# Kernel tuning notes

Measured on AMD Instinct MI355X. Metric: run time of the kernel, lower is better.

Reference implementation:

```python
import jax, jax.numpy as jnp
import numpy as np

B, E, H, NC = 16384, 1024, 8, 32
FF = 4 * E

def _ln(x, g, b, eps=1e-5):
    m = jnp.mean(x, -1, keepdims=True)
    v = jnp.mean((x - m) ** 2, -1, keepdims=True)
    return (x - m) * jax.lax.rsqrt(v + eps) * g + b

def _mha1(q_in, kv_in, Wq, Wk, Wv, bq, bk, bv, Wo, bo):
    # seq_len == 1 for both query and key/value; x: [B, E]
    Bn = q_in.shape[0]
    dh = E // H
    q = (q_in @ Wq.T + bq).reshape(Bn, H, dh)
    k = (kv_in @ Wk.T + bk).reshape(Bn, H, dh)
    v = (kv_in @ Wv.T + bv).reshape(Bn, H, dh)
    s = jnp.sum(q * k, -1, keepdims=True) / np.float32(np.sqrt(dh))  # [B,H,1]
    w = jax.nn.softmax(s, axis=-1)  # single key -> weights == 1 exactly
    o = (w * v).reshape(Bn, E)
    return o @ Wo.T + bo

def _ffn(x, W1, b1, W2, b2):
    h = jax.nn.gelu(x @ W1.T + b1, approximate=False)  # torch GELU = exact erf
    return h @ W2.T + b2

def setup_inputs():
    key = jax.random.key(0)
    ks = iter(jax.random.split(key, 64))
    def w(shape, s=0.02):
        return jax.random.normal(next(ks), shape, jnp.float32) * s
    z = lambda n: jnp.zeros((n,), jnp.float32)
    o = lambda n: jnp.ones((n,), jnp.float32)
    d = {
        'lc_cls': jax.random.normal(next(ks), (B, E), jnp.float32),
        'tab_embedding': jax.random.normal(next(ks), (B, E), jnp.float32),
        'ln_lc_g': o(E), 'ln_lc_b': z(E),
        'ln_tab_g': o(E), 'ln_tab_b': z(E),
    }
    for p in ('alc', 'atab'):
        d[p + '_Wq'] = w((E, E)); d[p + '_Wk'] = w((E, E)); d[p + '_Wv'] = w((E, E))
        d[p + '_bq'] = z(E); d[p + '_bk'] = z(E); d[p + '_bv'] = z(E)
        d[p + '_Wo'] = w((E, E)); d[p + '_bo'] = z(E)
    for p in ('flc', 'ftab'):
        d[p + '_W1'] = w((FF, E)); d[p + '_b1'] = z(FF)
        d[p + '_W2'] = w((E, FF)); d[p + '_b2'] = z(E)
    d['on_g'] = o(2 * E); d['on_b'] = z(2 * E)
    d['c_W1'] = w((E, 2 * E)); d['c_b1'] = z(E)
    d['c_ln_g'] = o(E); d['c_ln_b'] = z(E)
    d['c_W2'] = w((NC, E)); d['c_b2'] = z(NC)
    return d

def reference(lc_cls, tab_embedding, ln_lc_g, ln_lc_b, ln_tab_g, ln_tab_b,
              alc_Wq, alc_Wk, alc_Wv, alc_bq, alc_bk, alc_bv, alc_Wo, alc_bo,
              atab_Wq, atab_Wk, atab_Wv, atab_bq, atab_bk, atab_bv, atab_Wo, atab_bo,
              flc_W1, flc_b1, flc_W2, flc_b2, ftab_W1, ftab_b1, ftab_W2, ftab_b2,
              on_g, on_b, c_W1, c_b1, c_ln_g, c_ln_b, c_W2, c_b2):
    # dropout is identity at inference
    lc_n = _ln(lc_cls, ln_lc_g, ln_lc_b)
    tab_n = _ln(tab_embedding, ln_tab_g, ln_tab_b)
    lc_cross = lc_cls + _mha1(lc_n, tab_n, alc_Wq, alc_Wk, alc_Wv, alc_bq, alc_bk, alc_bv, alc_Wo, alc_bo)
    tab_cross = tab_embedding + _mha1(tab_n, lc_n, atab_Wq, atab_Wk, atab_Wv, atab_bq, atab_bk, atab_bv, atab_Wo, atab_bo)
    lc_out = lc_cross + _ffn(lc_cross, flc_W1, flc_b1, flc_W2, flc_b2)
    tab_out = tab_cross + _ffn(tab_cross, ftab_W1, ftab_b1, ftab_W2, ftab_b2)
    fused = _ln(jnp.concatenate([lc_out, tab_out], axis=1), on_g, on_b)
    h = jax.nn.gelu(_ln(fused @ c_W1.T + c_b1, c_ln_g, c_ln_b), approximate=False)
    return h @ c_W2.T + c_b2
```

## Files before the change

### kernel.cpp

```cpp
#include <hip/hip_runtime.h>
#include <hip/hip_bf16.h>
#include <math.h>

typedef __bf16 bf16_t;
typedef __bf16 bf16x8 __attribute__((ext_vector_type(8)));
typedef __bf16 bf16x4 __attribute__((ext_vector_type(4)));
typedef float  f32x4  __attribute__((ext_vector_type(4)));

#define NB   16384
#define EDIM 1024
#define FFD  4096
#define NCD  32

__device__ __forceinline__ float gelu_exact(float x) {
    return 0.5f * x * (1.0f + erff(x * 0.70710678118654752f));
}

__device__ __forceinline__ void gload16(const bf16_t* g, bf16_t* l) {
    __builtin_amdgcn_global_load_lds(
        (__attribute__((address_space(1))) void*)(g),
        (__attribute__((address_space(3))) void*)(l),
        16, 0, 0);
}

#define PH_BAR() do { asm volatile("" ::: "memory"); \
                      __builtin_amdgcn_s_barrier();  \
                      asm volatile("" ::: "memory"); } while (0)

enum { EPI_PLAIN = 0, EPI_RESF32 = 1, EPI_GELU = 2, EPI_RESBF16 = 3 };

struct GemmArgs {
    const bf16_t* A0; const bf16_t* A1;
    const bf16_t* B0; const bf16_t* B1;
    const float*  bias0; const float* bias1;
    const void*   res0; const void*  res1;
    bf16_t*       out0; bf16_t*      out1;
};

template<int EPI>
__global__ __launch_bounds__(256, 4)
void gemmDB(GemmArgs g, int ldo, int co0, int co1, int M, int N, int K)
{
    __shared__ __align__(128) bf16_t lds[16384];
    char* const ldsb = (char*)lds;

    const int side = blockIdx.z;
    const bf16_t* __restrict__ A    = side ? g.A1   : g.A0;
    const bf16_t* __restrict__ Bw   = side ? g.B1   : g.B0;
    const float*  __restrict__ bias = side ? g.bias1: g.bias0;
    const void*   __restrict__ resid= side ? g.res1 : g.res0;
    bf16_t*       __restrict__ out  = side ? g.out1 : g.out0;
    const int coloff = side ? co1 : co0;

    const int nx = gridDim.x;
    const int nwg = nx * gridDim.y;
    int lin = blockIdx.y * nx + blockIdx.x;
    {
        const int q = nwg >> 3, r = nwg & 7;
        const int xc = lin & 7, ix = lin >> 3;
        lin = (xc < r ? xc * (q + 1) : r * (q + 1) + (xc - r) * q) + ix;
    }
    const long bm = (long)(lin / nx) * 128;
    const long bn = (long)(lin % nx) * 128;

    const int tid = threadIdx.x, lane = tid & 63, wave = tid >> 6;
    const int wr = (wave >> 1) * 64, wc = (wave & 1) * 64;
    const int fr = lane & 15, ks = lane >> 4;
    const int fx = fr & 3;
    const int csw = (ks ^ fx) << 4;

    const int srow = lane >> 2;
    const int sl   = ((lane & 3) ^ ((lane >> 2) & 3)) * 8;
    auto STAGE = [&](const bf16_t* __restrict__ Mat, long row0, long kt,
                     int dsto) {
        #pragma unroll
        for (int i = 0; i < 2; ++i) {
            gload16(Mat + (row0 + i * 64 + wave * 16 + srow) * (long)K + kt + sl,
                    (bf16_t*)(ldsb + dsto + (i * 256 + wave * 64) * 16));
        }
    };

    f32x4 acc[4][4] = {};
    const int nt = K >> 5;

    STAGE(A,  bm, 0, 0);
    STAGE(Bw, bn, 0, 8192);
    asm volatile("s_waitcnt vmcnt(0)" ::: "memory");
    PH_BAR();

    for (int t = 0; t < nt; ++t) {
        const char* base = ldsb + (t & 1) * 16384;
        bf16x8 av[4], bv[4];
        #pragma unroll
        for (int i = 0; i < 4; ++i) {
            av[i] = *(const bf16x8*)(base + (wr + i * 16 + fr) * 64 + csw);
            bv[i] = *(const bf16x8*)(base + 8192 + (wc + i * 16 + fr) * 64 + csw);
        }
        if (t + 1 < nt) {
            const int nb = ((t + 1) & 1) * 16384;
            STAGE(A,  bm, (long)(t + 1) << 5, nb);
            STAGE(Bw, bn, (long)(t + 1) << 5, nb + 8192);
        }
        #pragma unroll
        for (int mi = 0; mi < 4; ++mi)
            #pragma unroll
            for (int ni = 0; ni < 4; ++ni)
                acc[mi][ni] = __builtin_amdgcn_mfma_f32_16x16x32_bf16(
                                  av[mi], bv[ni], acc[mi][ni], 0, 0, 0);
        asm volatile("s_waitcnt vmcnt(0)" ::: "memory");
        PH_BAR();
    }

    const int rq = (lane >> 4) * 4;
    #pragma unroll
    for (int mi = 0; mi < 4; ++mi) {
        #pragma unroll
        for (int ni = 0; ni < 4; ++ni) {
            const long n = bn + wc + ni * 16 + fr;
            const float bval = bias ? bias[n] : 0.0f;
            #pragma unroll
            for (int r = 0; r < 4; ++r) {
                const long m = bm + wr + mi * 16 + rq + r;
                float v = acc[mi][ni][r] + bval;
                if (EPI == EPI_RESF32)  v += ((const float*)resid)[m * (long)N + n];
                if (EPI == EPI_RESBF16) v += (float)((const bf16_t*)resid)[m * (long)N + n];
                if (EPI == EPI_GELU)    v = gelu_exact(v);
                out[m * (long)ldo + coloff + n] = (bf16_t)v;
            }
        }
    }
}

__global__ __launch_bounds__(256)
void final_mfma(const bf16_t* __restrict__ U, const bf16_t* __restrict__ W2,
                const float* __restrict__ b2, float* __restrict__ out)
{
    __shared__ bf16_t sA[128 * 32];
    __shared__ bf16_t sB[32 * 32];
    const int tid = threadIdx.x, lane = tid & 63, wave = tid >> 6;
    const long bm = (long)blockIdx.x * 128;
    const int srow = lane >> 2, scol = (lane & 3) * 8;

    const bf16_t* gA = U + (bm + wave * 32 + srow) * (long)EDIM + scol;
    bf16_t* lA = sA + wave * 32 * 32;
    const bf16_t* gB = W2 + ((long)wave * 16 + srow) * EDIM + scol;
    bf16_t* lB = sB + wave * 16 * 32;

    const int fr = lane & 15, fk = (lane >> 4) * 8;
    const bf16_t* rA = sA + (wave * 32 + fr) * 32 + fk;
    const bf16_t* rB = sB + fr * 32 + fk;

    f32x4 acc[2][2] = {};
    for (int kt = 0; kt < EDIM; kt += 32) {
        gload16(gA + kt,             lA);
        gload16(gA + kt + 16 * EDIM, lA + 16 * 32);
        if (wave < 2) gload16(gB + kt, lB);
        __syncthreads();
        bf16x8 av[2], bv[2];
        av[0] = *(const bf16x8*)(rA);
        av[1] = *(const bf16x8*)(rA + 16 * 32);
        bv[0] = *(const bf16x8*)(rB);
        bv[1] = *(const bf16x8*)(rB + 16 * 32);
        #pragma unroll
        for (int mi = 0; mi < 2; ++mi)
            #pragma unroll
            for (int ni = 0; ni < 2; ++ni)
                acc[mi][ni] = __builtin_amdgcn_mfma_f32_16x16x32_bf16(
                                  av[mi], bv[ni], acc[mi][ni], 0, 0, 0);
        __syncthreads();
    }
    const int rq = (lane >> 4) * 4;
    #pragma unroll
    for (int mi = 0; mi < 2; ++mi)
        #pragma unroll
        for (int ni = 0; ni < 2; ++ni) {
            const int n = ni * 16 + fr;
            const float bval = b2[n];
            #pragma unroll
            for (int r = 0; r < 4; ++r) {
                const long m = bm + wave * 32 + mi * 16 + rq + r;
                out[m * NCD + n] = acc[mi][ni][r] + bval;
            }
        }
}

__global__ __launch_bounds__(256)
void ln_f32(const float* __restrict__ X, const float* __restrict__ g,
            const float* __restrict__ b, bf16_t* __restrict__ out)
{
    const long row = blockIdx.x;
    const int t = threadIdx.x;
    f32x4 x = ((const f32x4*)(X + row * EDIM))[t];
    float s = x[0] + x[1] + x[2] + x[3];
    float q = x[0]*x[0] + x[1]*x[1] + x[2]*x[2] + x[3]*x[3];
    #pragma unroll
    for (int off = 32; off; off >>= 1) { s += __shfl_xor(s, off); q += __shfl_xor(q, off); }
    __shared__ float red[8];
    if ((t & 63) == 0) { red[(t >> 6) * 2] = s; red[(t >> 6) * 2 + 1] = q; }
    __syncthreads();
    s = red[0] + red[2] + red[4] + red[6];
    q = red[1] + red[3] + red[5] + red[7];
    const float mean = s * (1.0f / EDIM);
    const float rs = rsqrtf(q * (1.0f / EDIM) - mean * mean + 1e-5f);
    f32x4 gg = ((const f32x4*)g)[t];
    f32x4 bb = ((const f32x4*)b)[t];
    bf16x4 o;
    #pragma unroll
    for (int j = 0; j < 4; ++j) o[j] = (bf16_t)((x[j] - mean) * rs * gg[j] + bb[j]);
    ((bf16x4*)(out + row * EDIM))[t] = o;
}

__global__ __launch_bounds__(256)
void ln_cat(const bf16_t* __restrict__ X, const float* __restrict__ g,
            const float* __restrict__ b, bf16_t* __restrict__ out)
{
    const long row = blockIdx.x;
    const int t = threadIdx.x;
    bf16x8 xv = ((const bf16x8*)(X + row * 2048))[t];
    float xf[8];
    float s = 0.f, q = 0.f;
    #pragma unroll
    for (int j = 0; j < 8; ++j) { xf[j] = (float)xv[j]; s += xf[j]; q += xf[j] * xf[j]; }
    #pragma unroll
    for (int off = 32; off; off >>= 1) { s += __shfl_xor(s, off); q += __shfl_xor(q, off); }
    __shared__ float red[8];
    if ((t & 63) == 0) { red[(t >> 6) * 2] = s; red[(t >> 6) * 2 + 1] = q; }
    __syncthreads();
    s = red[0] + red[2] + red[4] + red[6];
    q = red[1] + red[3] + red[5] + red[7];
    const float mean = s * (1.0f / 2048);
    const float rs = rsqrtf(q * (1.0f / 2048) - mean * mean + 1e-5f);
    f32x4 g0 = ((const f32x4*)g)[2 * t], g1 = ((const f32x4*)g)[2 * t + 1];
    f32x4 b0 = ((const f32x4*)b)[2 * t], b1 = ((const f32x4*)b)[2 * t + 1];
    bf16x8 o;
    #pragma unroll
    for (int j = 0; j < 4; ++j) o[j]     = (bf16_t)((xf[j]     - mean) * rs * g0[j] + b0[j]);
    #pragma unroll
    for (int j = 0; j < 4; ++j) o[4 + j] = (bf16_t)((xf[4 + j] - mean) * rs * g1[j] + b1[j]);
    ((bf16x8*)(out + row * 2048))[t] = o;
}

__global__ __launch_bounds__(256)
void ln_gelu(const bf16_t* __restrict__ X, const float* __restrict__ g,
             const float* __restrict__ b, bf16_t* __restrict__ out)
{
    const long row = blockIdx.x;
    const int t = threadIdx.x;
    bf16x4 xv = ((const bf16x4*)(X + row * EDIM))[t];
    float xf[4];
    float s = 0.f, q = 0.f;
    #pragma unroll
    for (int j = 0; j < 4; ++j) { xf[j] = (float)xv[j]; s += xf[j]; q += xf[j] * xf[j]; }
    #pragma unroll
    for (int off = 32; off; off >>= 1) { s += __shfl_xor(s, off); q += __shfl_xor(q, off); }
    __shared__ float red[8];
    if ((t & 63) == 0) { red[(t >> 6) * 2] = s; red[(t >> 6) * 2 + 1] = q; }
    __syncthreads();
    s = red[0] + red[2] + red[4] + red[6];
    q = red[1] + red[3] + red[5] + red[7];
    const float mean = s * (1.0f / EDIM);
    const float rs = rsqrtf(q * (1.0f / EDIM) - mean * mean + 1e-5f);
    f32x4 gg = ((const f32x4*)g)[t];
    f32x4 bb = ((const f32x4*)b)[t];
    bf16x4 o;
    #pragma unroll
    for (int j = 0; j < 4; ++j)
        o[j] = (bf16_t)gelu_exact((xf[j] - mean) * rs * gg[j] + bb[j]);
    ((bf16x4*)(out + row * EDIM))[t] = o;
}

__global__ void f2b(const float* __restrict__ in, bf16_t* __restrict__ out, long n4)
{
    long i = (long)blockIdx.x * blockDim.x + threadIdx.x;
    const long stride = (long)gridDim.x * blockDim.x;
    for (; i < n4; i += stride) {
        f32x4 v = ((const f32x4*)in)[i];
        bf16x4 o;
        #pragma unroll
        for (int j = 0; j < 4; ++j) o[j] = (bf16_t)v[j];
        ((bf16x4*)out)[i] = o;
    }
}

__global__ void tconv(const float* __restrict__ in, bf16_t* __restrict__ out)
{
    const long x = (long)blockIdx.x * 256 + threadIdx.x;
    const int k = (int)(x & (EDIM - 1));
    const int j = (int)(x >> 10);
    out[(long)j * EDIM + k] = (bf16_t)in[(long)k * EDIM + j];
}

__global__ __launch_bounds__(256)
void bcomb_k(const float* __restrict__ Wo, const float* __restrict__ bv,
             const float* __restrict__ bo, float* __restrict__ bc)
{
    const int i = blockIdx.x;
    const int t = threadIdx.x;
    f32x4 w = ((const f32x4*)(Wo + (long)i * EDIM))[t];
    f32x4 v = ((const f32x4*)bv)[t];
    float s = w[0]*v[0] + w[1]*v[1] + w[2]*v[2] + w[3]*v[3];
    #pragma unroll
    for (int off = 32; off; off >>= 1) s += __shfl_xor(s, off);
    __shared__ float red[4];
    if ((t & 63) == 0) red[t >> 6] = s;
    __syncthreads();
    if (t == 0) bc[i] = red[0] + red[1] + red[2] + red[3] + bo[i];
}

extern "C" void kernel_launch(void* const* d_in, const int* in_sizes, int n_in,
                              void* d_out, int out_size, void* d_ws, size_t ws_size,
                              hipStream_t stream)
{
    const float* lc_cls   = (const float*)d_in[0];
    const float* tab_emb  = (const float*)d_in[1];
    const float* ln_lc_g  = (const float*)d_in[2];
    const float* ln_lc_b  = (const float*)d_in[3];
    const float* ln_tab_g = (const float*)d_in[4];
    const float* ln_tab_b = (const float*)d_in[5];
    const float* alc_Wv   = (const float*)d_in[8];
    const float* alc_bv   = (const float*)d_in[11];
    const float* alc_Wo   = (const float*)d_in[12];
    const float* alc_bo   = (const float*)d_in[13];
    const float* atab_Wv  = (const float*)d_in[16];
    const float* atab_bv  = (const float*)d_in[19];
    const float* atab_Wo  = (const float*)d_in[20];
    const float* atab_bo  = (const float*)d_in[21];
    const float* flc_W1   = (const float*)d_in[22];
    const float* flc_b1   = (const float*)d_in[23];
    const float* flc_W2   = (const float*)d_in[24];
    const float* flc_b2   = (const float*)d_in[25];
    const float* ftab_W1  = (const float*)d_in[26];
    const float* ftab_b1  = (const float*)d_in[27];
    const float* ftab_W2  = (const float*)d_in[28];
    const float* ftab_b2  = (const float*)d_in[29];
    const float* on_g     = (const float*)d_in[30];
    const float* on_b     = (const float*)d_in[31];
    const float* c_W1     = (const float*)d_in[32];
    const float* c_b1     = (const float*)d_in[33];
    const float* c_ln_g   = (const float*)d_in[34];
    const float* c_ln_b   = (const float*)d_in[35];
    const float* c_W2     = (const float*)d_in[36];
    const float* c_b2     = (const float*)d_in[37];

    char* ws = (char*)d_ws;
    size_t woff = 0;
    auto walloc = [&](size_t bytes) {
        void* p = ws + woff;
        woff += (bytes + 255) & ~(size_t)255;
        return p;
    };
    bf16_t* Wc_lc  = (bf16_t*)walloc((size_t)EDIM * EDIM * 2);
    bf16_t* Wc_tab = (bf16_t*)walloc((size_t)EDIM * EDIM * 2);
    bf16_t* W1lc_b = (bf16_t*)walloc((size_t)FFD * EDIM * 2);
    bf16_t* W2lc_b = (bf16_t*)walloc((size_t)EDIM * FFD * 2);
    bf16_t* W1tab_b= (bf16_t*)walloc((size_t)FFD * EDIM * 2);
    bf16_t* W2tab_b= (bf16_t*)walloc((size_t)EDIM * FFD * 2);
    bf16_t* cW1_b  = (bf16_t*)walloc((size_t)EDIM * 2 * EDIM * 2);
    bf16_t* cW2_b  = (bf16_t*)walloc((size_t)NCD * EDIM * 2);
    float*  bc_lc  = (float*)walloc(EDIM * 4);
    float*  bc_tab = (float*)walloc(EDIM * 4);

    char* arena = ws + woff;
    const size_t arena_sz = (ws_size > woff) ? (ws_size - woff) : 0;

    int SB = NB;
    while (SB > 256 && (size_t)SB * 24576 > arena_sz) SB >>= 1;
    if ((size_t)SB * 24576 > arena_sz) return;

    const size_t S2 = (size_t)SB * 2048;
    bf16_t* lc_n  = (bf16_t*)(arena);
    bf16_t* tab_n = (bf16_t*)(arena + S2);
    bf16_t* cat   = (bf16_t*)(arena);
    bf16_t* lc_x  = (bf16_t*)(arena + 2 * S2);
    bf16_t* tab_x = (bf16_t*)(arena + 3 * S2);
    bf16_t* hbuf0 = (bf16_t*)(arena + 4 * S2);
    bf16_t* hbuf1 = (bf16_t*)(arena + 8 * S2);
    bf16_t* tbuf  = lc_x;
    bf16_t* ubuf  = tab_x;

    bf16_t* Wo_lc_b  = (bf16_t*)(arena);
    bf16_t* Wo_tab_b = (bf16_t*)(arena + (size_t)2 * 1024 * 1024);
    bf16_t* WvT_lc   = (bf16_t*)(arena + (size_t)4 * 1024 * 1024);
    bf16_t* WvT_tab  = (bf16_t*)(arena + (size_t)6 * 1024 * 1024);

    f2b<<<512, 256, 0, stream>>>(alc_Wo,  Wo_lc_b,  (long)EDIM * EDIM / 4);
    f2b<<<512, 256, 0, stream>>>(atab_Wo, Wo_tab_b, (long)EDIM * EDIM / 4);
    tconv<<<EDIM * EDIM / 256, 256, 0, stream>>>(alc_Wv,  WvT_lc);
    tconv<<<EDIM * EDIM / 256, 256, 0, stream>>>(atab_Wv, WvT_tab);
    f2b<<<2048, 256, 0, stream>>>(flc_W1,  W1lc_b,  (long)FFD * EDIM / 4);
    f2b<<<2048, 256, 0, stream>>>(flc_W2,  W2lc_b,  (long)EDIM * FFD / 4);
    f2b<<<2048, 256, 0, stream>>>(ftab_W1, W1tab_b, (long)FFD * EDIM / 4);
    f2b<<<2048, 256, 0, stream>>>(ftab_W2, W2tab_b, (long)EDIM * FFD / 4);
    f2b<<<1024, 256, 0, stream>>>(c_W1,    cW1_b,   (long)EDIM * 2 * EDIM / 4);
    f2b<<<32,   256, 0, stream>>>(c_W2,    cW2_b,   (long)NCD * EDIM / 4);
    bcomb_k<<<EDIM, 256, 0, stream>>>(alc_Wo,  alc_bv,  alc_bo,  bc_lc);
    bcomb_k<<<EDIM, 256, 0, stream>>>(atab_Wo, atab_bv, atab_bo, bc_tab);
    {
        GemmArgs ga = { Wo_lc_b, Wo_tab_b, WvT_lc, WvT_tab,
                        nullptr, nullptr, nullptr, nullptr, Wc_lc, Wc_tab };
        gemmDB<EPI_PLAIN><<<dim3(EDIM/128, EDIM/128, 2), 256, 0, stream>>>(
            ga, EDIM, 0, 0, EDIM, EDIM, EDIM);
    }

    for (long c0 = 0; c0 < NB; c0 += SB) {
        const float* lcI  = lc_cls  + c0 * EDIM;
        const float* tabI = tab_emb + c0 * EDIM;

        ln_f32<<<SB, 256, 0, stream>>>(lcI,  ln_lc_g,  ln_lc_b,  lc_n);
        ln_f32<<<SB, 256, 0, stream>>>(tabI, ln_tab_g, ln_tab_b, tab_n);

        {
            GemmArgs ga = { tab_n, lc_n, Wc_lc, Wc_tab, bc_lc, bc_tab,
                            lcI, tabI, lc_x, tab_x };
            gemmDB<EPI_RESF32><<<dim3(EDIM/128, SB/128, 2), 256, 0, stream>>>(
                ga, EDIM, 0, 0, SB, EDIM, EDIM);
        }
        {
            GemmArgs ga = { lc_x, tab_x, W1lc_b, W1tab_b, flc_b1, ftab_b1,
                            nullptr, nullptr, hbuf0, hbuf1 };
            gemmDB<EPI_GELU><<<dim3(FFD/128, SB/128, 2), 256, 0, stream>>>(
                ga, FFD, 0, 0, SB, FFD, EDIM);
        }
        {
            GemmArgs ga = { hbuf0, hbuf1, W2lc_b, W2tab_b, flc_b2, ftab_b2,
                            lc_x, tab_x, cat, cat };
            gemmDB<EPI_RESBF16><<<dim3(EDIM/128, SB/128, 2), 256, 0, stream>>>(
                ga, 2 * EDIM, 0, EDIM, SB, EDIM, FFD);
        }

        ln_cat<<<SB, 256, 0, stream>>>(cat, on_g, on_b, cat);

        {
            GemmArgs ga = { cat, cat, cW1_b, cW1_b, c_b1, c_b1,
                            nullptr, nullptr, tbuf, tbuf };
            gemmDB<EPI_PLAIN><<<dim3(EDIM/128, SB/128, 1), 256, 0, stream>>>(
                ga, EDIM, 0, 0, SB, EDIM, 2 * EDIM);
        }
        ln_gelu<<<SB, 256, 0, stream>>>(tbuf, c_ln_g, c_ln_b, ubuf);
        final_mfma<<<SB / 128, 256, 0, stream>>>(ubuf, cW2_b, c_b2,
                                                 (float*)d_out + c0 * NCD);
    }
}
```

Before: 1.167 ms.

## Widen GEMM tile to 256x128 with 512 threads and triple-buffered LDS pipeline

Replaces the double-buffered 128x128 GEMM with a 256x128 tile computed by 8 waves, sharing each staged B tile across twice as many rows. LDS becomes a three-stage ring, so loads run two k-steps ahead and each step waits only for the oldest stage instead of draining all outstanding loads. The cost is 72KB of LDS per block, which limits how many blocks fit per CU, and half as many blocks per launch.

```diff
diff --git a/kernel.cpp b/kernel.cpp
--- a/kernel.cpp
+++ b/kernel.cpp
@@ -38,10 +38,10 @@
 };
 
 template<int EPI>
-__global__ __launch_bounds__(256, 4)
-void gemmDB(GemmArgs g, int ldo, int co0, int co1, int M, int N, int K)
-{
-    __shared__ __align__(128) bf16_t lds[16384];
+__global__ __launch_bounds__(512, 4)
+void gemmP2(GemmArgs g, int ldo, int co0, int co1, int M, int N, int K)
+{
+    __shared__ __align__(128) bf16_t lds[36864];
     char* const ldsb = (char*)lds;
 
     const int side = blockIdx.z;
@@ -60,54 +60,54 @@
         const int xc = lin & 7, ix = lin >> 3;
         lin = (xc < r ? xc * (q + 1) : r * (q + 1) + (xc - r) * q) + ix;
     }
-    const long bm = (long)(lin / nx) * 128;
+    const long bm = (long)(lin / nx) * 256;
     const long bn = (long)(lin % nx) * 128;
 
     const int tid = threadIdx.x, lane = tid & 63, wave = tid >> 6;
-    const int wr = (wave >> 1) * 64, wc = (wave & 1) * 64;
+    const int wm = wave >> 1, wn = wave & 1;
     const int fr = lane & 15, ks = lane >> 4;
-    const int fx = fr & 3;
-    const int csw = (ks ^ fx) << 4;
-
-    const int srow = lane >> 2;
-    const int sl   = ((lane & 3) ^ ((lane >> 2) & 3)) * 8;
-    auto STAGE = [&](const bf16_t* __restrict__ Mat, long row0, long kt,
-                     int dsto) {
-        #pragma unroll
-        for (int i = 0; i < 2; ++i) {
-            gload16(Mat + (row0 + i * 64 + wave * 16 + srow) * (long)K + kt + sl,
-                    (bf16_t*)(ldsb + dsto + (i * 256 + wave * 64) * 16));
-        }
+    const int csw = ((ks ^ (fr & 3)) << 4);
+
+    const int sl = ((tid & 3) ^ ((tid >> 2) & 3)) * 8;
+    const bf16_t* gA = A  + (bm + (tid >> 2)) * (long)K + sl;
+    const bf16_t* gB = Bw + (bn + (tid >> 2)) * (long)K + sl;
+    bf16_t* const dA0 = (bf16_t*)(ldsb + wave * 1024);
+    bf16_t* const dA1 = (bf16_t*)(ldsb + 8192  + wave * 1024);
+    bf16_t* const dB  = (bf16_t*)(ldsb + 16384 + wave * 1024);
+
+    const int nt = K >> 5;
+    auto STAGE = [&](int t) {
+        const int bufo = (t % 3) * 24576;
+        const long kt = (long)t << 5;
+        gload16(gA + kt,                 (bf16_t*)((char*)dA0 + bufo));
+        gload16(gA + kt + 128 * (long)K, (bf16_t*)((char*)dA1 + bufo));
+        gload16(gB + kt,                 (bf16_t*)((char*)dB  + bufo));
     };
 
     f32x4 acc[4][4] = {};
-    const int nt = K >> 5;
-
-    STAGE(A,  bm, 0, 0);
-    STAGE(Bw, bn, 0, 8192);
-    asm volatile("s_waitcnt vmcnt(0)" ::: "memory");
+
+    STAGE(0);
+    STAGE(1);
+    asm volatile("s_waitcnt vmcnt(3)" ::: "memory");
     PH_BAR();
 
     for (int t = 0; t < nt; ++t) {
-        const char* base = ldsb + (t & 1) * 16384;
+        const char* base = ldsb + (t % 3) * 24576;
         bf16x8 av[4], bv[4];
         #pragma unroll
         for (int i = 0; i < 4; ++i) {
-            av[i] = *(const bf16x8*)(base + (wr + i * 16 + fr) * 64 + csw);
-            bv[i] = *(const bf16x8*)(base + 8192 + (wc + i * 16 + fr) * 64 + csw);
-        }
-        if (t + 1 < nt) {
-            const int nb = ((t + 1) & 1) * 16384;
-            STAGE(A,  bm, (long)(t + 1) << 5, nb);
-            STAGE(Bw, bn, (long)(t + 1) << 5, nb + 8192);
-        }
+            av[i] = *(const bf16x8*)(base + (wm * 64 + i * 16 + fr) * 64 + csw);
+            bv[i] = *(const bf16x8*)(base + 16384 + (wn * 64 + i * 16 + fr) * 64 + csw);
+        }
+        if (t + 2 < nt) STAGE(t + 2);
         #pragma unroll
         for (int mi = 0; mi < 4; ++mi)
             #pragma unroll
             for (int ni = 0; ni < 4; ++ni)
                 acc[mi][ni] = __builtin_amdgcn_mfma_f32_16x16x32_bf16(
                                   av[mi], bv[ni], acc[mi][ni], 0, 0, 0);
-        asm volatile("s_waitcnt vmcnt(0)" ::: "memory");
+        if (t + 2 < nt) { asm volatile("s_waitcnt vmcnt(3)" ::: "memory"); }
+        else            { asm volatile("s_waitcnt vmcnt(0)" ::: "memory"); }
         PH_BAR();
     }
 
@@ -116,11 +116,11 @@
     for (int mi = 0; mi < 4; ++mi) {
         #pragma unroll
         for (int ni = 0; ni < 4; ++ni) {
-            const long n = bn + wc + ni * 16 + fr;
+            const long n = bn + wn * 64 + ni * 16 + fr;
             const float bval = bias ? bias[n] : 0.0f;
             #pragma unroll
             for (int r = 0; r < 4; ++r) {
-                const long m = bm + wr + mi * 16 + rq + r;
+                const long m = bm + wm * 64 + mi * 16 + rq + r;
                 float v = acc[mi][ni][r] + bval;
                 if (EPI == EPI_RESF32)  v += ((const float*)resid)[m * (long)N + n];
                 if (EPI == EPI_RESBF16) v += (float)((const bf16_t*)resid)[m * (long)N + n];
@@ -398,7 +398,7 @@
     {
         GemmArgs ga = { Wo_lc_b, Wo_tab_b, WvT_lc, WvT_tab,
                         nullptr, nullptr, nullptr, nullptr, Wc_lc, Wc_tab };
-        gemmDB<EPI_PLAIN><<<dim3(EDIM/128, EDIM/128, 2), 256, 0, stream>>>(
+        gemmP2<EPI_PLAIN><<<dim3(EDIM/128, EDIM/256, 2), 512, 0, stream>>>(
             ga, EDIM, 0, 0, EDIM, EDIM, EDIM);
     }
 
@@ -412,19 +412,19 @@
         {
             GemmArgs ga = { tab_n, lc_n, Wc_lc, Wc_tab, bc_lc, bc_tab,
                             lcI, tabI, lc_x, tab_x };
-            gemmDB<EPI_RESF32><<<dim3(EDIM/128, SB/128, 2), 256, 0, stream>>>(
+            gemmP2<EPI_RESF32><<<dim3(EDIM/128, SB/256, 2), 512, 0, stream>>>(
                 ga, EDIM, 0, 0, SB, EDIM, EDIM);
         }
         {
             GemmArgs ga = { lc_x, tab_x, W1lc_b, W1tab_b, flc_b1, ftab_b1,
                             nullptr, nullptr, hbuf0, hbuf1 };
-            gemmDB<EPI_GELU><<<dim3(FFD/128, SB/128, 2), 256, 0, stream>>>(
+            gemmP2<EPI_GELU><<<dim3(FFD/128, SB/256, 2), 512, 0, stream>>>(
                 ga, FFD, 0, 0, SB, FFD, EDIM);
         }
         {
             GemmArgs ga = { hbuf0, hbuf1, W2lc_b, W2tab_b, flc_b2, ftab_b2,
                             lc_x, tab_x, cat, cat };
-            gemmDB<EPI_RESBF16><<<dim3(EDIM/128, SB/128, 2), 256, 0, stream>>>(
+            gemmP2<EPI_RESBF16><<<dim3(EDIM/128, SB/256, 2), 512, 0, stream>>>(
                 ga, 2 * EDIM, 0, EDIM, SB, EDIM, FFD);
         }
 
@@ -433,7 +433,7 @@
         {
             GemmArgs ga = { cat, cat, cW1_b, cW1_b, c_b1, c_b1,
                             nullptr, nullptr, tbuf, tbuf };
-            gemmDB<EPI_PLAIN><<<dim3(EDIM/128, SB/128, 1), 256, 0, stream>>>(
+            gemmP2<EPI_PLAIN><<<dim3(EDIM/128, SB/256, 1), 512, 0, stream>>>(
                 ga, EDIM, 0, 0, SB, EDIM, 2 * EDIM);
         }
         ln_gelu<<<SB, 256, 0, stream>>>(tbuf, c_ln_g, c_ln_b, ubuf);
```

Result: faster. 1.058 ms (-9.3%).
